# Performance work log

Hardware: AMD Instinct MI355X
Metric: run time of the kernel (lower is better)

Reference implementation:

```python
import jax, jax.numpy as jnp
import numpy as np
from jax import lax

N_PTS = 256          # hardcoded point count in original loops
BIG = 257.0 ** 2     # initial SE sentinel in original code


def setup_inputs() -> dict:
    key = jax.random.key(0)
    k1, k2 = jax.random.split(key)
    B = 2048
    inp = jax.random.normal(k1, (B, 1, 2 * N_PTS), dtype=jnp.float32)
    tgt = jax.random.normal(k2, (B, 1, 2 * N_PTS), dtype=jnp.float32)
    return {"input": inp, "targets": tgt}


def reference(input, targets):
    B = input.shape[0]
    # interleaved (x, y) pairs -> [B, 256, 2]
    pin = input[:, 0, :].reshape(B, N_PTS, 2)
    ptg = targets[:, 0, :].reshape(B, N_PTS, 2)
    # pairwise squared distances: D[b, j, k] = ||tgt_j - in_k||^2
    D = jnp.sum((ptg[:, :, None, :] - pin[:, None, :, :]) ** 2, axis=-1)  # [B,256,256]
    big = jnp.asarray(BIG, dtype=D.dtype)
    batch_idx = jnp.arange(B)

    def step(used, dj):
        # dj: [B, 256] distances from target point j to all input points
        vals = jnp.where(used, jnp.inf, dj)
        m = jnp.min(vals, axis=1)
        k = jnp.argmin(vals, axis=1)
        se = jnp.minimum(m, big)              # SE stays 257^2 if nothing beats it
        k = jnp.where(m < big, k, 0)          # k_tmp stays 0 in that case
        used = used.at[batch_idx, k].set(True)
        return used, se

    used0 = jnp.zeros((B, N_PTS), dtype=bool)
    _, ses = lax.scan(step, used0, jnp.swapaxes(D, 0, 1))  # iterate j=0..255, ses: [256, B]
    loss = jnp.sum(ses) / B / (2 * N_PTS)
    return loss
```

## Files before the change

### kernel.cpp

```cpp
#include <hip/hip_runtime.h>
#include <stdint.h>

#define N_PTS 256

typedef unsigned long long ull;
typedef float v2f __attribute__((ext_vector_type(2)));

__device__ __forceinline__ unsigned umin2(unsigned a, unsigned b) { return a < b ? a : b; }

template<int CTRL>
__device__ __forceinline__ float dpp_min1(float x) {
    int xi = __float_as_int(x);
    int yi = __builtin_amdgcn_update_dpp(xi, xi, CTRL, 0xf, 0xf, false);
    return fminf(x, __int_as_float(yi));
}

__device__ __forceinline__ void round_one(
    float tjx, float tjy, int lane, float& acc,
    v2f& p0, v2f& p1, v2f& p2, v2f& p3)
{
    #pragma clang fp contract(off)
    const unsigned BIG_U = __float_as_uint(66049.0f);

    v2f t; t.x = tjx; t.y = tjy;
    v2f q0 = t - p0, q1 = t - p1, q2 = t - p2, q3 = t - p3;
    v2f s0 = q0 * q0, s1 = q1 * q1, s2 = q2 * q2, s3 = q3 * q3;
    float d0 = s0.x + s0.y;
    float d1 = s1.x + s1.y;
    float d2 = s2.x + s2.y;
    float d3 = s3.x + s3.y;

    float m = fminf(fminf(fminf(d0, d1), d2), d3);
    m = dpp_min1<0x111>(m);
    m = dpp_min1<0x112>(m);
    m = dpp_min1<0x114>(m);
    m = dpp_min1<0x118>(m);
    unsigned r0 = (unsigned)__builtin_amdgcn_readlane(__float_as_int(m), 15);
    unsigned r1 = (unsigned)__builtin_amdgcn_readlane(__float_as_int(m), 31);
    unsigned r2 = (unsigned)__builtin_amdgcn_readlane(__float_as_int(m), 47);
    unsigned r3 = (unsigned)__builtin_amdgcn_readlane(__float_as_int(m), 63);
    unsigned mu = umin2(umin2(r0, r1), umin2(r2, r3));
    float mf = __uint_as_float(mu);

    ull e0 = __ballot(d0 == mf);
    ull e1 = __ballot(d1 == mf);
    ull e2 = __ballot(d2 == mf);
    ull e3 = __ballot(d3 == mf);
    unsigned u0 = (unsigned)(__ffsll((long long)e0) - 1);
    unsigned u1 = (unsigned)((__ffsll((long long)e1) - 1) | 64);
    unsigned u2 = (unsigned)((__ffsll((long long)e2) - 1) | 128);
    unsigned u3 = (unsigned)((__ffsll((long long)e3) - 1) | 192);
    unsigned k  = umin2(umin2(u0, u1), umin2(u2, u3));

    bool ok = (mu < BIG_U);
    k  = ok ? k : 0u;
    mu = umin2(mu, BIG_U);
    acc += __uint_as_float(mu);

    const float NANF = __int_as_float(0x7fc00000);
    const unsigned ks = k >> 6, kl = k & 63u;
    const bool hit = ((unsigned)lane == kl);
    p0.x = (hit && ks == 0) ? NANF : p0.x;
    p1.x = (hit && ks == 1) ? NANF : p1.x;
    p2.x = (hit && ks == 2) ? NANF : p2.x;
    p3.x = (hit && ks == 3) ? NANF : p3.x;
}

__device__ __forceinline__ void greedy_phase(
    float txc, float tyc, int lane, float& acc,
    v2f& p0, v2f& p1, v2f& p2, v2f& p3)
{
    #pragma unroll 1
    for (int j2 = 0; j2 < 64; ++j2) {
        float tjx = __int_as_float(__builtin_amdgcn_readlane(__float_as_int(txc), j2));
        float tjy = __int_as_float(__builtin_amdgcn_readlane(__float_as_int(tyc), j2));
        round_one(tjx, tjy, lane, acc, p0, p1, p2, p3);
    }
}

__global__ __launch_bounds__(256) void greedy_match_kernel(
    const float* __restrict__ input,
    const float* __restrict__ targets,
    float* __restrict__ out,
    int B, float scale)
{
    __shared__ float wsum[4];
    const int lane = threadIdx.x & 63;
    const int wid  = threadIdx.x >> 6;
    const int b    = blockIdx.x * 4 + wid;

    float acc = 0.0f;
    if (b < B) {
        const v2f* pin = (const v2f*)(input   + (size_t)b * (2 * N_PTS));
        const v2f* ptg = (const v2f*)(targets + (size_t)b * (2 * N_PTS));

        v2f p0 = pin[lane];
        v2f p1 = pin[64 + lane];
        v2f p2 = pin[128 + lane];
        v2f p3 = pin[192 + lane];
        v2f t0 = ptg[lane];
        v2f t1 = ptg[64 + lane];
        v2f t2 = ptg[128 + lane];
        v2f t3 = ptg[192 + lane];

        greedy_phase(t0.x, t0.y, lane, acc, p0, p1, p2, p3);
        greedy_phase(t1.x, t1.y, lane, acc, p0, p1, p2, p3);
        greedy_phase(t2.x, t2.y, lane, acc, p0, p1, p2, p3);
        greedy_phase(t3.x, t3.y, lane, acc, p0, p1, p2, p3);
    }

    if (lane == 0) wsum[wid] = acc;
    __syncthreads();
    if (threadIdx.x == 0) {
        float s = (wsum[0] + wsum[1] + wsum[2] + wsum[3]) * scale;
        atomicAdd(out, s);
    }
}

extern "C" void kernel_launch(void* const* d_in, const int* in_sizes, int n_in,
                              void* d_out, int out_size, void* d_ws, size_t ws_size,
                              hipStream_t stream) {
    const float* input   = (const float*)d_in[0];
    const float* targets = (const float*)d_in[1];
    float* out = (float*)d_out;

    const int B = in_sizes[0] / (2 * N_PTS);
    const float scale = 1.0f / ((float)B * (float)(2 * N_PTS));

    hipMemsetAsync(d_out, 0, sizeof(float) * (size_t)out_size, stream);

    const int blocks = (B + 3) / 4;
    greedy_match_kernel<<<blocks, 256, 0, stream>>>(input, targets, out, B, scale);
}
```

Measured before the change: 130.5 us.

## Interleave two batch rows per wave and replace ballot argmin with DPP reduction

Each wavefront now runs two independent greedy matchings, one per batch row, interleaved inside the same loop. This gives the scheduler independent instruction chains to hide the latency of the serial DPP and readlane reductions. The min reduction is finished with row-broadcast DPP steps and a single readlane. The index search now uses a second DPP min-reduction over per-lane candidate indices instead of four ballots and ffs. The cost is half as many blocks (1024 waves for B=2048) and more registers per thread, which can reduce occupancy and the number of waves available across CUs.

```diff
diff --git a/kernel.cpp b/kernel.cpp
--- a/kernel.cpp
+++ b/kernel.cpp
@@ -3,25 +3,29 @@
 
 #define N_PTS 256
 
-typedef unsigned long long ull;
 typedef float v2f __attribute__((ext_vector_type(2)));
 
-__device__ __forceinline__ unsigned umin2(unsigned a, unsigned b) { return a < b ? a : b; }
+template<int CTRL>
+__device__ __forceinline__ float dppmin_f(float x) {
+    int xi = __float_as_int(x);
+    int yi = __builtin_amdgcn_update_dpp(xi, xi, CTRL, 0xf, 0xf, false);
+    float y = __int_as_float(yi);
+    return fminf(x, y);
+}
 
 template<int CTRL>
-__device__ __forceinline__ float dpp_min1(float x) {
-    int xi = __float_as_int(x);
-    int yi = __builtin_amdgcn_update_dpp(xi, xi, CTRL, 0xf, 0xf, false);
-    return fminf(x, __int_as_float(yi));
+__device__ __forceinline__ unsigned dppmin_u(unsigned x) {
+    unsigned y = (unsigned)__builtin_amdgcn_update_dpp((int)x, (int)x, CTRL, 0xf, 0xf, false);
+    return x < y ? x : y;
 }
 
-__device__ __forceinline__ void round_one(
+__device__ __forceinline__ void round1(
     float tjx, float tjy, int lane, float& acc,
-    v2f& p0, v2f& p1, v2f& p2, v2f& p3)
+    v2f& p0, v2f& p1, v2f& p2, v2f& p3,
+    unsigned vL0, unsigned vL64, unsigned vL128, unsigned vL192,
+    unsigned vBAD, float vNAN)
 {
     #pragma clang fp contract(off)
-    const unsigned BIG_U = __float_as_uint(66049.0f);
-
     v2f t; t.x = tjx; t.y = tjy;
     v2f q0 = t - p0, q1 = t - p1, q2 = t - p2, q3 = t - p3;
     v2f s0 = q0 * q0, s1 = q1 * q1, s2 = q2 * q2, s3 = q3 * q3;
@@ -31,50 +35,57 @@
     float d3 = s3.x + s3.y;
 
     float m = fminf(fminf(fminf(d0, d1), d2), d3);
-    m = dpp_min1<0x111>(m);
-    m = dpp_min1<0x112>(m);
-    m = dpp_min1<0x114>(m);
-    m = dpp_min1<0x118>(m);
-    unsigned r0 = (unsigned)__builtin_amdgcn_readlane(__float_as_int(m), 15);
-    unsigned r1 = (unsigned)__builtin_amdgcn_readlane(__float_as_int(m), 31);
-    unsigned r2 = (unsigned)__builtin_amdgcn_readlane(__float_as_int(m), 47);
-    unsigned r3 = (unsigned)__builtin_amdgcn_readlane(__float_as_int(m), 63);
-    unsigned mu = umin2(umin2(r0, r1), umin2(r2, r3));
-    float mf = __uint_as_float(mu);
+    m = dppmin_f<0x111>(m);
+    m = dppmin_f<0x112>(m);
+    m = dppmin_f<0x114>(m);
+    m = dppmin_f<0x118>(m);
+    m = dppmin_f<0x142>(m);
+    m = dppmin_f<0x143>(m);
+    unsigned mu = (unsigned)__builtin_amdgcn_readlane(__float_as_int(m), 63);
+    float ms = __uint_as_float(mu);
 
-    ull e0 = __ballot(d0 == mf);
-    ull e1 = __ballot(d1 == mf);
-    ull e2 = __ballot(d2 == mf);
-    ull e3 = __ballot(d3 == mf);
-    unsigned u0 = (unsigned)(__ffsll((long long)e0) - 1);
-    unsigned u1 = (unsigned)((__ffsll((long long)e1) - 1) | 64);
-    unsigned u2 = (unsigned)((__ffsll((long long)e2) - 1) | 128);
-    unsigned u3 = (unsigned)((__ffsll((long long)e3) - 1) | 192);
-    unsigned k  = umin2(umin2(u0, u1), umin2(u2, u3));
+    unsigned u = (d0 == ms) ? vL0
+               : (d1 == ms) ? vL64
+               : (d2 == ms) ? vL128
+               : (d3 == ms) ? vL192
+               : vBAD;
+    u = dppmin_u<0x111>(u);
+    u = dppmin_u<0x112>(u);
+    u = dppmin_u<0x114>(u);
+    u = dppmin_u<0x118>(u);
+    u = dppmin_u<0x142>(u);
+    u = dppmin_u<0x143>(u);
+    unsigned k = (unsigned)__builtin_amdgcn_readlane((int)u, 63);
 
+    const unsigned BIG_U = __float_as_uint(66049.0f);
     bool ok = (mu < BIG_U);
-    k  = ok ? k : 0u;
-    mu = umin2(mu, BIG_U);
-    acc += __uint_as_float(mu);
+    k = ok ? k : 0u;
+    unsigned se = (mu < BIG_U) ? mu : BIG_U;
+    acc += __uint_as_float(se);
 
-    const float NANF = __int_as_float(0x7fc00000);
-    const unsigned ks = k >> 6, kl = k & 63u;
-    const bool hit = ((unsigned)lane == kl);
-    p0.x = (hit && ks == 0) ? NANF : p0.x;
-    p1.x = (hit && ks == 1) ? NANF : p1.x;
-    p2.x = (hit && ks == 2) ? NANF : p2.x;
-    p3.x = (hit && ks == 3) ? NANF : p3.x;
+    unsigned ks = k >> 6, kl = k & 63u;
+    bool hit = ((unsigned)lane == kl);
+    p0.x = (hit && ks == 0) ? vNAN : p0.x;
+    p1.x = (hit && ks == 1) ? vNAN : p1.x;
+    p2.x = (hit && ks == 2) ? vNAN : p2.x;
+    p3.x = (hit && ks == 3) ? vNAN : p3.x;
 }
 
-__device__ __forceinline__ void greedy_phase(
-    float txc, float tyc, int lane, float& acc,
-    v2f& p0, v2f& p1, v2f& p2, v2f& p3)
+__device__ __forceinline__ void phase2(
+    float txX, float tyX, float txY, float tyY, int lane,
+    float& accX, v2f& x0, v2f& x1, v2f& x2, v2f& x3,
+    float& accY, v2f& y0, v2f& y1, v2f& y2, v2f& y3,
+    unsigned vL0, unsigned vL64, unsigned vL128, unsigned vL192,
+    unsigned vBAD, float vNAN)
 {
     #pragma unroll 1
-    for (int j2 = 0; j2 < 64; ++j2) {
-        float tjx = __int_as_float(__builtin_amdgcn_readlane(__float_as_int(txc), j2));
-        float tjy = __int_as_float(__builtin_amdgcn_readlane(__float_as_int(tyc), j2));
-        round_one(tjx, tjy, lane, acc, p0, p1, p2, p3);
+    for (int j = 0; j < 64; ++j) {
+        float aX = __int_as_float(__builtin_amdgcn_readlane(__float_as_int(txX), j));
+        float bX = __int_as_float(__builtin_amdgcn_readlane(__float_as_int(tyX), j));
+        float aY = __int_as_float(__builtin_amdgcn_readlane(__float_as_int(txY), j));
+        float bY = __int_as_float(__builtin_amdgcn_readlane(__float_as_int(tyY), j));
+        round1(aX, bX, lane, accX, x0, x1, x2, x3, vL0, vL64, vL128, vL192, vBAD, vNAN);
+        round1(aY, bY, lane, accY, y0, y1, y2, y3, vL0, vL64, vL128, vL192, vBAD, vNAN);
     }
 }
 
@@ -87,29 +98,41 @@
     __shared__ float wsum[4];
     const int lane = threadIdx.x & 63;
     const int wid  = threadIdx.x >> 6;
-    const int b    = blockIdx.x * 4 + wid;
+    const int bX   = blockIdx.x * 8 + wid * 2;
+    const int bY   = bX + 1;
+    const bool vX  = (bX < B), vY = (bY < B);
+    const int cX   = vX ? bX : 0;
+    const int cY   = vY ? bY : 0;
 
-    float acc = 0.0f;
-    if (b < B) {
-        const v2f* pin = (const v2f*)(input   + (size_t)b * (2 * N_PTS));
-        const v2f* ptg = (const v2f*)(targets + (size_t)b * (2 * N_PTS));
+    const v2f* pinX = (const v2f*)(input   + (size_t)cX * (2 * N_PTS));
+    const v2f* ptgX = (const v2f*)(targets + (size_t)cX * (2 * N_PTS));
+    const v2f* pinY = (const v2f*)(input   + (size_t)cY * (2 * N_PTS));
+    const v2f* ptgY = (const v2f*)(targets + (size_t)cY * (2 * N_PTS));
 
-        v2f p0 = pin[lane];
-        v2f p1 = pin[64 + lane];
-        v2f p2 = pin[128 + lane];
-        v2f p3 = pin[192 + lane];
-        v2f t0 = ptg[lane];
-        v2f t1 = ptg[64 + lane];
-        v2f t2 = ptg[128 + lane];
-        v2f t3 = ptg[192 + lane];
+    v2f x0 = pinX[lane], x1 = pinX[64 + lane], x2 = pinX[128 + lane], x3 = pinX[192 + lane];
+    v2f tX0 = ptgX[lane], tX1 = ptgX[64 + lane], tX2 = ptgX[128 + lane], tX3 = ptgX[192 + lane];
+    v2f y0 = pinY[lane], y1 = pinY[64 + lane], y2 = pinY[128 + lane], y3 = pinY[192 + lane];
+    v2f tY0 = ptgY[lane], tY1 = ptgY[64 + lane], tY2 = ptgY[128 + lane], tY3 = ptgY[192 + lane];
 
-        greedy_phase(t0.x, t0.y, lane, acc, p0, p1, p2, p3);
-        greedy_phase(t1.x, t1.y, lane, acc, p0, p1, p2, p3);
-        greedy_phase(t2.x, t2.y, lane, acc, p0, p1, p2, p3);
-        greedy_phase(t3.x, t3.y, lane, acc, p0, p1, p2, p3);
-    }
+    const unsigned vL0   = (unsigned)lane;
+    const unsigned vL64  = vL0 | 64u;
+    const unsigned vL128 = vL0 | 128u;
+    const unsigned vL192 = vL0 | 192u;
+    const unsigned vBAD  = 1023u;
+    const float    vNAN  = __int_as_float(0x7fc00000);
 
-    if (lane == 0) wsum[wid] = acc;
+    float accX = 0.0f, accY = 0.0f;
+    phase2(tX0.x, tX0.y, tY0.x, tY0.y, lane, accX, x0, x1, x2, x3,
+           accY, y0, y1, y2, y3, vL0, vL64, vL128, vL192, vBAD, vNAN);
+    phase2(tX1.x, tX1.y, tY1.x, tY1.y, lane, accX, x0, x1, x2, x3,
+           accY, y0, y1, y2, y3, vL0, vL64, vL128, vL192, vBAD, vNAN);
+    phase2(tX2.x, tX2.y, tY2.x, tY2.y, lane, accX, x0, x1, x2, x3,
+           accY, y0, y1, y2, y3, vL0, vL64, vL128, vL192, vBAD, vNAN);
+    phase2(tX3.x, tX3.y, tY3.x, tY3.y, lane, accX, x0, x1, x2, x3,
+           accY, y0, y1, y2, y3, vL0, vL64, vL128, vL192, vBAD, vNAN);
+
+    float a = (vX ? accX : 0.0f) + (vY ? accY : 0.0f);
+    if (lane == 0) wsum[wid] = a;
     __syncthreads();
     if (threadIdx.x == 0) {
         float s = (wsum[0] + wsum[1] + wsum[2] + wsum[3]) * scale;
@@ -129,6 +152,6 @@
 
     hipMemsetAsync(d_out, 0, sizeof(float) * (size_t)out_size, stream);
 
-    const int blocks = (B + 3) / 4;
+    const int blocks = (B + 7) / 8;
     greedy_match_kernel<<<blocks, 256, 0, stream>>>(input, targets, out, B, scale);
 }
```

Result: slower. 191.1 us (+46.5%).
